# Performance work log

Hardware: AMD Instinct MI355X
Metric: run time of the kernel (lower is better)

Reference implementation:

```python
import jax, jax.numpy as jnp
import numpy as np

GROUPS = 4
GROUP_SIZE = 64
NORMED = True


def setup_inputs() -> dict:
    key = jax.random.key(0)
    k1, k2 = jax.random.split(key)
    x = jax.random.normal(k1, (2, 4096, 4096), dtype=jnp.float32)
    # weight: [groups*group_out, group_in] = [4096, 1024], init std 0.02 as in torch
    weight = jax.random.normal(k2, (4096, 1024), dtype=jnp.float32) * 0.02
    return {"x": x, "weight": weight}


def reference(x, weight):
    if NORMED:
        # F.rms_norm with eps=None uses finfo(dtype).eps
        eps = jnp.finfo(x.dtype).eps
        x = x * jax.lax.rsqrt(jnp.mean(x * x, axis=-1, keepdims=True) + eps)

    # bf16 cast of weight (matches torch `.bfloat16()`), quantize in flat chunks of GROUP_SIZE
    w = weight.astype(jnp.bfloat16)
    w_g = w.reshape(-1, GROUP_SIZE)
    scale = jnp.clip(jnp.mean(jnp.abs(w_g), axis=-1, keepdims=True), 1e-8, None)
    q = jnp.clip(jnp.round(w_g / scale), -1.0, 1.0)
    # STE: forward value is q*scale, gradient flows through w
    w_ternary = w + jax.lax.stop_gradient((q * scale).reshape(w.shape) - w)

    group_in = weight.shape[1]
    group_out = weight.shape[0] // GROUPS
    w_grouped = w_ternary.reshape(GROUPS, group_out, group_in)

    bsz = x.shape[:-1]
    x_g = x.reshape(bsz + (GROUPS, group_in))
    # block-diagonal grouped matmul; promote bf16 weight to x dtype (exact upcast)
    out = jnp.einsum('...gi,goi->...go', x_g, w_grouped.astype(x.dtype))
    return out.reshape(bsz + (GROUPS * group_out,))
```

## Files before the change

kernel.cpp:

```cpp
#include <hip/hip_runtime.h>
#include <hip/hip_bf16.h>
#include <stdint.h>

__device__ __forceinline__ unsigned short f2bf(float f) {
    __hip_bfloat16 h = __float2bfloat16(f);
    return *reinterpret_cast<unsigned short*>(&h);
}
__device__ __forceinline__ float bf2f(unsigned short u) {
    __hip_bfloat16 h = *reinterpret_cast<__hip_bfloat16*>(&u);
    return __bfloat162float(h);
}

typedef __attribute__((ext_vector_type(8))) short bf16x8;
typedef __attribute__((ext_vector_type(4))) float f32x4;

__device__ __forceinline__ void async16(const void* g, void* l) {
    __builtin_amdgcn_global_load_lds(
        (const __attribute__((address_space(1))) unsigned int*)g,
        (__attribute__((address_space(3))) unsigned int*)l,
        16, 0, 0);
}

__global__ __launch_bounds__(256) void quant_kernel(const float* __restrict__ W,
                                                    unsigned short* __restrict__ Wq) {
    int idx = blockIdx.x * 256 + threadIdx.x;
    float wf = W[idx];
    float wbf = bf2f(f2bf(wf));
    float a = fabsf(wbf);
    float s = a;
    #pragma unroll
    for (int off = 32; off; off >>= 1) s += __shfl_xor(s, off, 64);
    float mean = s * (1.0f / 64.0f);
    float sf = bf2f(f2bf(mean));
    sf = fmaxf(sf, 1.0011718e-08f);
    float quot = bf2f(f2bf(wbf / sf));
    float q = rintf(quot);
    q = fminf(1.0f, fmaxf(-1.0f, q));
    float qs = q * sf;
    float d  = bf2f(f2bf(qs - wbf));
    Wq[idx] = f2bf(wbf + d);
}

__global__ __launch_bounds__(256) void norm_kernel(const float* __restrict__ X,
                                                   unsigned short* __restrict__ Xb) {
    __shared__ float red[4];
    const long long row = blockIdx.x;
    const float4* xr = (const float4*)(X + row * 4096);
    const int t = threadIdx.x;
    float4 v[4];
    float ss = 0.f;
    #pragma unroll
    for (int i = 0; i < 4; ++i) {
        v[i] = xr[i * 256 + t];
        ss += v[i].x * v[i].x + v[i].y * v[i].y + v[i].z * v[i].z + v[i].w * v[i].w;
    }
    #pragma unroll
    for (int off = 32; off; off >>= 1) ss += __shfl_xor(ss, off, 64);
    if ((t & 63) == 0) red[t >> 6] = ss;
    __syncthreads();
    const float tot = red[0] + red[1] + red[2] + red[3];
    const float scale = 1.0f / sqrtf(tot * (1.0f / 4096.0f) + 1.1920928955078125e-07f);
    ushort4* ob = (ushort4*)(Xb + row * 4096);
    #pragma unroll
    for (int i = 0; i < 4; ++i) {
        ushort4 o;
        o.x = f2bf(v[i].x * scale);
        o.y = f2bf(v[i].y * scale);
        o.z = f2bf(v[i].z * scale);
        o.w = f2bf(v[i].w * scale);
        ob[i * 256 + t] = o;
    }
}

#define BK 64
__global__ __launch_bounds__(256, 2) void gemm_kernel(const unsigned short* __restrict__ Xb,
                                                      const unsigned short* __restrict__ Wq,
                                                      float* __restrict__ Out) {
    __shared__ unsigned short lsA[128 * BK];
    __shared__ unsigned short lsB[128 * BK];

    const int t = threadIdx.x;
    const int lane = t & 63;
    const int wv = t >> 6;
    const int wr = wv >> 1, wc = wv & 1;

    const int bm0 = (blockIdx.x & 63) * 128;
    const int bn0 = (blockIdx.x >> 6) * 128;
    const int g = bn0 >> 10;
    const long long abase = (long long)bm0 * 4096 + g * 1024;

    f32x4 acc[4][4];
    #pragma unroll
    for (int i = 0; i < 4; ++i)
        #pragma unroll
        for (int j = 0; j < 4; ++j) acc[i][j] = (f32x4){0.f, 0.f, 0.f, 0.f};

    const int srow = t >> 3;
    const int scol = (t & 7) * 8;

    for (int kt = 0; kt < 1024 / BK; ++kt) {
        const int k0 = kt * BK;
        #pragma unroll
        for (int c = 0; c < 4; ++c) {
            const unsigned short* gp = Xb + abase + (long long)(c * 32 + srow) * 4096 + k0 + scol;
            async16(gp, (char*)lsA + c * 4096 + t * 16);
        }
        #pragma unroll
        for (int c = 0; c < 4; ++c) {
            const unsigned short* gp = Wq + (long long)(bn0 + c * 32 + srow) * 1024 + k0 + scol;
            async16(gp, (char*)lsB + c * 4096 + t * 16);
        }
        __syncthreads();

        #pragma unroll
        for (int ks = 0; ks < 2; ++ks) {
            bf16x8 afr[4], bfr[4];
            const int kk = ks * 32 + (lane >> 4) * 8;
            #pragma unroll
            for (int mi = 0; mi < 4; ++mi) {
                const int row = wr * 64 + mi * 16 + (lane & 15);
                afr[mi] = *(const bf16x8*)&lsA[row * BK + kk];
            }
            #pragma unroll
            for (int ni = 0; ni < 4; ++ni) {
                const int row = wc * 64 + ni * 16 + (lane & 15);
                bfr[ni] = *(const bf16x8*)&lsB[row * BK + kk];
            }
            #pragma unroll
            for (int mi = 0; mi < 4; ++mi)
                #pragma unroll
                for (int ni = 0; ni < 4; ++ni)
                    acc[mi][ni] = __builtin_amdgcn_mfma_f32_16x16x32_bf16(afr[mi], bfr[ni], acc[mi][ni], 0, 0, 0);
        }
        __syncthreads();
    }

    #pragma unroll
    for (int mi = 0; mi < 4; ++mi) {
        #pragma unroll
        for (int ni = 0; ni < 4; ++ni) {
            const int col = bn0 + wc * 64 + ni * 16 + (lane & 15);
            const int rowb = bm0 + wr * 64 + mi * 16 + (lane >> 4) * 4;
            #pragma unroll
            for (int r = 0; r < 4; ++r)
                Out[(long long)(rowb + r) * 4096 + col] = acc[mi][ni][r];
        }
    }
}

extern "C" void kernel_launch(void* const* d_in, const int* in_sizes, int n_in,
                              void* d_out, int out_size, void* d_ws, size_t ws_size,
                              hipStream_t stream) {
    const float* x = (const float*)d_in[0];
    const float* w = (const float*)d_in[1];
    float* out = (float*)d_out;

    unsigned short* xb = (unsigned short*)d_ws;
    unsigned short* wq = xb + (size_t)8192 * 4096;

    quant_kernel<<<4096 * 1024 / 256, 256, 0, stream>>>(w, wq);
    norm_kernel<<<8192, 256, 0, stream>>>(x, xb);
    gemm_kernel<<<2048, 256, 0, stream>>>(xb, wq, out);
}
```

Measured before the change: 336.9 us.

## Rewrite GEMM as 256x256 tile with 4-stage async LDS pipeline and swizzle

The grouped GEMM moves from 128x128 tiles with single-buffered BK=64 loads to 256x256 tiles, 512 threads and a 4-deep ring of BK=32 LDS buffers filled three steps ahead with async global-to-LDS loads. It adds an XOR swizzle on LDS columns to avoid bank conflicts, block-index swizzling for L2 locality, s_setprio around MFMA bursts, and explicit vmcnt waits in place of full syncthreads. The aim is to hide global-load latency behind MFMA work and raise data reuse per tile. The cost is higher register pressure (32 accumulator fragments per wave) and only 512 blocks, which may leave some CUs idle on a 256-CU part.

```diff
diff --git a/kernel.cpp b/kernel.cpp
--- a/kernel.cpp
+++ b/kernel.cpp
@@ -72,75 +72,106 @@
     }
 }
 
-#define BK 64
-__global__ __launch_bounds__(256, 2) void gemm_kernel(const unsigned short* __restrict__ Xb,
+__global__ __launch_bounds__(512, 2) void gemm_kernel(const unsigned short* __restrict__ Xb,
                                                       const unsigned short* __restrict__ Wq,
                                                       float* __restrict__ Out) {
-    __shared__ unsigned short lsA[128 * BK];
-    __shared__ unsigned short lsB[128 * BK];
+    __shared__ unsigned short lsA[4][256 * 32];
+    __shared__ unsigned short lsB[4][256 * 32];
 
-    const int t = threadIdx.x;
-    const int lane = t & 63;
-    const int wv = t >> 6;
-    const int wr = wv >> 1, wc = wv & 1;
+    const int tid = threadIdx.x;
+    const int lane = tid & 63;
+    const int wv = tid >> 6;
+    const int wr = wv >> 2;
+    const int wc = wv & 3;
 
-    const int bm0 = (blockIdx.x & 63) * 128;
-    const int bn0 = (blockIdx.x >> 6) * 128;
+    const int bid = blockIdx.x;
+    const int swz = (bid & 7) * 64 + (bid >> 3);
+    const int bm0 = (swz & 31) * 256;
+    const int bn0 = (swz >> 5) * 256;
     const int g = bn0 >> 10;
-    const long long abase = (long long)bm0 * 4096 + g * 1024;
 
-    f32x4 acc[4][4];
+    const int srow = tid >> 2;
+    const int cswz = (tid & 3) ^ ((tid >> 3) & 3);
+    const unsigned short* pA0 = Xb + (long long)(bm0 + srow) * 4096 + g * 1024 + cswz * 8;
+    const unsigned short* pA1 = pA0 + (long long)128 * 4096;
+    const unsigned short* pB0 = Wq + (long long)(bn0 + srow) * 1024 + cswz * 8;
+    const unsigned short* pB1 = pB0 + (long long)128 * 1024;
+    const int ldst = tid * 8;
+
+    const int cb = (lane >> 4) ^ ((lane >> 1) & 3);
+    const int aOff = (wr * 128 + (lane & 15)) * 32 + cb * 8;
+    const int bOff = (wc * 64 + (lane & 15)) * 32 + cb * 8;
+
+    f32x4 acc[8][4];
     #pragma unroll
-    for (int i = 0; i < 4; ++i)
+    for (int i = 0; i < 8; ++i)
         #pragma unroll
         for (int j = 0; j < 4; ++j) acc[i][j] = (f32x4){0.f, 0.f, 0.f, 0.f};
 
-    const int srow = t >> 3;
-    const int scol = (t & 7) * 8;
+    const int T = 32;
 
-    for (int kt = 0; kt < 1024 / BK; ++kt) {
-        const int k0 = kt * BK;
-        #pragma unroll
-        for (int c = 0; c < 4; ++c) {
-            const unsigned short* gp = Xb + abase + (long long)(c * 32 + srow) * 4096 + k0 + scol;
-            async16(gp, (char*)lsA + c * 4096 + t * 16);
-        }
-        #pragma unroll
-        for (int c = 0; c < 4; ++c) {
-            const unsigned short* gp = Wq + (long long)(bn0 + c * 32 + srow) * 1024 + k0 + scol;
-            async16(gp, (char*)lsB + c * 4096 + t * 16);
-        }
-        __syncthreads();
+    #pragma unroll
+    for (int pt = 0; pt < 3; ++pt) {
+        async16(pA0 + pt * 32, &lsA[pt][ldst]);
+        async16(pA1 + pt * 32, &lsA[pt][ldst + 4096]);
+        async16(pB0 + pt * 32, &lsB[pt][ldst]);
+        async16(pB1 + pt * 32, &lsB[pt][ldst + 4096]);
+    }
+    asm volatile("s_waitcnt vmcnt(8)" ::: "memory");
+    __builtin_amdgcn_s_barrier();
+
+    for (int t = 0; t < T; ++t) {
+        const unsigned short* sA = lsA[t & 3];
+        const unsigned short* sB = lsB[t & 3];
+        bf16x8 afr[4], bfr[4];
 
         #pragma unroll
-        for (int ks = 0; ks < 2; ++ks) {
-            bf16x8 afr[4], bfr[4];
-            const int kk = ks * 32 + (lane >> 4) * 8;
+        for (int ni = 0; ni < 4; ++ni) bfr[ni] = *(const bf16x8*)&sB[bOff + ni * 512];
+        #pragma unroll
+        for (int i = 0; i < 4; ++i) afr[i] = *(const bf16x8*)&sA[aOff + i * 512];
+        if (t + 3 < T) {
+            unsigned short* dA = lsA[(t + 3) & 3];
+            async16(pA0 + (t + 3) * 32, dA + ldst);
+            async16(pA1 + (t + 3) * 32, dA + ldst + 4096);
+        }
+        __builtin_amdgcn_s_barrier();
+        __builtin_amdgcn_s_setprio(1);
+        #pragma unroll
+        for (int i = 0; i < 4; ++i)
             #pragma unroll
-            for (int mi = 0; mi < 4; ++mi) {
-                const int row = wr * 64 + mi * 16 + (lane & 15);
-                afr[mi] = *(const bf16x8*)&lsA[row * BK + kk];
-            }
+            for (int ni = 0; ni < 4; ++ni)
+                acc[i][ni] = __builtin_amdgcn_mfma_f32_16x16x32_bf16(afr[i], bfr[ni], acc[i][ni], 0, 0, 0);
+        __builtin_amdgcn_s_setprio(0);
+        __builtin_amdgcn_s_barrier();
+
+        #pragma unroll
+        for (int i = 0; i < 4; ++i) afr[i] = *(const bf16x8*)&sA[aOff + (i + 4) * 512];
+        if (t + 3 < T) {
+            unsigned short* dB = lsB[(t + 3) & 3];
+            async16(pB0 + (t + 3) * 32, dB + ldst);
+            async16(pB1 + (t + 3) * 32, dB + ldst + 4096);
+        }
+        __builtin_amdgcn_s_barrier();
+        __builtin_amdgcn_s_setprio(1);
+        #pragma unroll
+        for (int i = 0; i < 4; ++i)
             #pragma unroll
-            for (int ni = 0; ni < 4; ++ni) {
-                const int row = wc * 64 + ni * 16 + (lane & 15);
-                bfr[ni] = *(const bf16x8*)&lsB[row * BK + kk];
-            }
-            #pragma unroll
-            for (int mi = 0; mi < 4; ++mi)
-                #pragma unroll
-                for (int ni = 0; ni < 4; ++ni)
-                    acc[mi][ni] = __builtin_amdgcn_mfma_f32_16x16x32_bf16(afr[mi], bfr[ni], acc[mi][ni], 0, 0, 0);
-        }
-        __syncthreads();
+            for (int ni = 0; ni < 4; ++ni)
+                acc[i + 4][ni] = __builtin_amdgcn_mfma_f32_16x16x32_bf16(afr[i], bfr[ni], acc[i + 4][ni], 0, 0, 0);
+        __builtin_amdgcn_s_setprio(0);
+
+        if (t < T - 3)       asm volatile("s_waitcnt vmcnt(8)" ::: "memory");
+        else if (t == T - 3) asm volatile("s_waitcnt vmcnt(4)" ::: "memory");
+        else if (t == T - 2) asm volatile("s_waitcnt vmcnt(0)" ::: "memory");
+        __builtin_amdgcn_s_barrier();
     }
 
     #pragma unroll
-    for (int mi = 0; mi < 4; ++mi) {
+    for (int mi = 0; mi < 8; ++mi) {
         #pragma unroll
         for (int ni = 0; ni < 4; ++ni) {
             const int col = bn0 + wc * 64 + ni * 16 + (lane & 15);
-            const int rowb = bm0 + wr * 64 + mi * 16 + (lane >> 4) * 4;
+            const int rowb = bm0 + wr * 128 + mi * 16 + (lane >> 4) * 4;
             #pragma unroll
             for (int r = 0; r < 4; ++r)
                 Out[(long long)(rowb + r) * 4096 + col] = acc[mi][ni][r];
@@ -160,5 +191,5 @@
 
     quant_kernel<<<4096 * 1024 / 256, 256, 0, stream>>>(w, wq);
     norm_kernel<<<8192, 256, 0, stream>>>(x, xb);
-    gemm_kernel<<<2048, 256, 0, stream>>>(xb, wq, out);
+    gemm_kernel<<<512, 512, 0, stream>>>(xb, wq, out);
 }
```

After: 336.1 us. No clear change (-0.2%).
